# Kernel tuning notes

Hardware: AMD Instinct MI355X
Metric: run time of the kernel (lower is better)

Reference implementation:

```python
import jax, jax.numpy as jnp
import numpy as np

NUM_BINS = 10
BIN_DISP = 0.5
MIN_REG = 1e-5
H = 22
W = 22
S = 16
C = 256
F_ = H * W


def _distance_map(center, sz):
    # DiMP DistanceMap: soft-binned radial distance from center. [bins, sz0, sz1]
    bins = jnp.arange(NUM_BINS, dtype=jnp.float32)[:, None, None]
    k0 = jnp.arange(sz[0], dtype=jnp.float32)[:, None]
    k1 = jnp.arange(sz[1], dtype=jnp.float32)[None, :]
    dist = jnp.sqrt((k0 - center[0]) ** 2 + (k1 - center[1]) ** 2)
    bd = dist[None] / BIN_DISP - bins
    lower = jax.nn.relu(1.0 - jnp.abs(bd[:-1]))
    last = jnp.clip(1.0 + bd[-1:], 0.0, 1.0)
    return jnp.concatenate([lower, last], axis=0)


def _unfold_map(fm, h, w):
    # Equivalent of F.unfold(full_map,(h,w)).view(h,w,h,w).flip((2,3)).permute(2,3,0,1):
    # out[f=(li,lj), ki, kj] = fm[h-1-li+ki, w-1-lj+kj]
    r = (h - 1 - jnp.arange(h))[:, None] + jnp.arange(h)[None, :]  # [li, ki]
    c = (w - 1 - jnp.arange(w))[:, None] + jnp.arange(w)[None, :]  # [lj, kj]
    m = fm[r[:, None, :, None], c[None, :, None, :]]  # [li, lj, ki, kj]
    return m.reshape(h * w, h, w)


def setup_inputs() -> dict:
    key = jax.random.key(0)
    k1, k2 = jax.random.split(key)
    filt = jax.random.normal(k1, (S, F_, C, 1, 1), jnp.float32) * 0.1
    feat = jax.random.normal(k2, (1, S, C, H, W), jnp.float32)
    d = jnp.arange(NUM_BINS, dtype=jnp.float32) * BIN_DISP
    init_gauss = jnp.exp(-0.5 * d ** 2)  # init_gauss_sigma = 1.0
    return {
        "filt": filt,
        "feat": feat,
        "log_step_length": jnp.zeros((1,), jnp.float32),          # log(1.0)
        "filter_reg": 0.01 * jnp.ones((1,), jnp.float32),
        "label_w": init_gauss - init_gauss.min(),                  # label_map_predictor weights
        "mask_w": 4.0 * jnp.tanh(2.0 - d),                         # target_mask_predictor weights
        "spatial_w": jnp.ones((NUM_BINS,), jnp.float32),           # spatial_weight_predictor weights
        "num_iter": 3,
    }


def _forward(filt, feat, log_step_length, filter_reg, label_w, mask_w, spatial_w, num_iter):
    f2 = feat[0]            # [S, C, H, W]
    w = filt[..., 0, 0]     # [S, F, C]   (1x1 DiCor filters)
    h, wd = feat.shape[-2], feat.shape[-1]
    s, fnum = w.shape[0], w.shape[1]
    sz = (2 * h - 1, 2 * wd - 1)
    center = jnp.array([sz[0] // 2, sz[1] // 2], dtype=jnp.float32)
    dmap = _distance_map(center, sz)  # [bins, 2H-1, 2W-1]
    # 1x1 convs over the bin dimension, then unfold into per-filter maps [F, H, W]
    label_map = _unfold_map(jnp.einsum('bhw,b->hw', dmap, label_w), h, wd)
    target_mask = _unfold_map(jax.nn.sigmoid(jnp.einsum('bhw,b->hw', dmap, mask_w)), h, wd)
    spatial_weight = _unfold_map(jnp.einsum('bhw,b->hw', dmap, spatial_w), h, wd)
    step_length = jnp.exp(log_step_length[0])
    reg_weight = jnp.maximum(filter_reg[0] * filter_reg[0], MIN_REG ** 2)
    a = target_mask
    sw2 = spatial_weight * spatial_weight
    for _ in range(num_iter):
        # apply_filter with 1x1 filters: scores[s,f,h,w] = sum_c feat[s,c,h,w] * w[s,f,c]
        scores = jnp.einsum('schw,sfc->sfhw', f2, w)
        # LeakyReluPar / LeakyReluParDeriv with per-location slope a
        scores_act = 0.5 * (1.0 - a) * jnp.abs(scores) + 0.5 * (1.0 + a) * scores
        score_mask = 0.5 * (1.0 - a) * jnp.sign(scores) + 0.5 * (1.0 + a)
        residuals = score_mask * (sw2 * (scores_act - label_map))
        # apply_feat_transpose with 1x1 filters
        w_grad = jnp.einsum('sfhw,schw->sfc', residuals, f2) + reg_weight * w
        scores_grad = jnp.einsum('schw,sfc->sfhw', f2, w_grad)
        scores_grad = spatial_weight * (score_mask * scores_grad)
        alpha_num = jnp.sum(w_grad * w_grad, axis=2)  # [S, F]
        alpha_den = jnp.maximum(
            jnp.sum((scores_grad * scores_grad).reshape(s, fnum, -1), axis=2)
            + reg_weight * alpha_num, 1e-8)
        alpha = alpha_num / alpha_den
        w = w - step_length * alpha[..., None] * w_grad
    return w[..., None, None]  # [S, F, C, 1, 1]


def reference(filt, feat, log_step_length, filter_reg, label_w, mask_w, spatial_w, num_iter):
    return _forward(filt, feat, log_step_length, filter_reg, label_w, mask_w, spatial_w, num_iter)
```

## Files before the change

### kernel.cpp

```cpp
#include <hip/hip_runtime.h>
#include <math.h>
#include <stdint.h>

#define Ww 22
#define P_ 484
#define S_ 16
#define C_ 256
#define MP2 234256
#define TSZ 1849

typedef _Float16 f16x8 __attribute__((ext_vector_type(8)));
typedef _Float16 f16x4 __attribute__((ext_vector_type(4)));
typedef float f32x4 __attribute__((ext_vector_type(4)));

__device__ __forceinline__ void gld16(const _Float16* g, _Float16* lds) {
    auto* lp = (__attribute__((address_space(3))) uint32_t*)(uintptr_t)(lds);
    auto* gp = (const __attribute__((address_space(1))) uint32_t*)(uintptr_t)(g);
    __builtin_amdgcn_global_load_lds(gp, lp, 16, 0, 0);
}

__global__ void k_maps(const float* __restrict__ label_w, const float* __restrict__ mask_w,
                       const float* __restrict__ spatial_w, f32x4* __restrict__ map4t) {
    int idx = blockIdx.x * blockDim.x + threadIdx.x;
    if (idx >= TSZ) return;
    int dx = idx / 43 - 21, dy = idx % 43 - 21;
    float d = sqrtf((float)(dx * dx + dy * dy)) * 2.0f;
    float lab = 0.f, msk = 0.f, spw = 0.f;
#pragma unroll
    for (int b = 0; b < 9; ++b) {
        float wb = fmaxf(0.f, 1.f - fabsf(d - (float)b));
        lab += wb * label_w[b];
        msk += wb * mask_w[b];
        spw += wb * spatial_w[b];
    }
    float w9 = fminf(fmaxf(1.f + (d - 9.f), 0.f), 1.f);
    lab += w9 * label_w[9];
    msk += w9 * mask_w[9];
    spw += w9 * spatial_w[9];
    f32x4 o;
    o[0] = lab;
    o[1] = 1.f / (1.f + expf(-msk));
    o[2] = spw * spw;
    o[3] = spw;
    map4t[idx] = o;
}

__global__ __launch_bounds__(256) void k_winit(const float* __restrict__ filt,
                                               float* __restrict__ Wf, _Float16* __restrict__ Wh,
                                               float* __restrict__ num, float* __restrict__ den) {
    int t = threadIdx.x;
    int f = blockIdx.x * 4 + (t >> 6);
    int s = blockIdx.y;
    int c = (t & 63) * 4;
    size_t oh = ((size_t)(s * 512 + f)) * C_ + c;
    if (f < P_) {
        size_t o = ((size_t)(s * P_ + f)) * C_ + c;
        f32x4 v = *(const f32x4*)(filt + o);
        *(f32x4*)(Wf + o) = v;
        f16x4 h;
#pragma unroll
        for (int q = 0; q < 4; ++q) h[q] = (_Float16)v[q];
        *(f16x4*)(Wh + oh) = h;
        if ((t & 63) == 0) { num[s * P_ + f] = 0.f; den[s * P_ + f] = 0.f; }
    } else {
        f16x4 h = {};
        *(f16x4*)(Wh + oh) = h;
    }
}

__global__ __launch_bounds__(256) void k_trans(const float* __restrict__ feat,
                                               _Float16* __restrict__ f2h,
                                               _Float16* __restrict__ f2th) {
    int s = blockIdx.z;
    int p0 = blockIdx.x * 32, c0 = blockIdx.y * 32;
    int cc = threadIdx.x & 31, rr = threadIdx.x >> 5;
    __shared__ float tb[32][33];
#pragma unroll
    for (int q = 0; q < 4; ++q) {
        int c = c0 + rr + q * 8;
        int p = p0 + cc;
        float v = (p < P_) ? feat[((size_t)s * C_ + c) * P_ + p] : 0.f;
        f2h[((size_t)s * C_ + c) * 512 + p] = (_Float16)v;
        tb[rr + q * 8][cc] = v;
    }
    __syncthreads();
#pragma unroll
    for (int q = 0; q < 4; ++q) {
        int p = p0 + rr + q * 8;
        f2th[((size_t)s * 512 + p) * C_ + c0 + cc] = (_Float16)tb[cc][rr + q * 8];
    }
}

template <int EPI, int KK, int LDA, int LDB>
__global__ __launch_bounds__(256, 4) void k_gemm(
    const _Float16* __restrict__ Ah, const _Float16* __restrict__ Bh,
    const f32x4* __restrict__ map4t, const _Float16* __restrict__ maskh_i,
    const _Float16* __restrict__ Wh_i, const float* __restrict__ freg,
    _Float16* __restrict__ out_h, _Float16* __restrict__ out_h2,
    float* __restrict__ red) {
    constexpr int TI = 2, TJ = 2, NT = KK / 128;
    int tid = threadIdx.x;
    int w = tid >> 6, l = tid & 63;
    int s = blockIdx.x;
    int m0 = blockIdx.y * 64, n0 = blockIdx.z * 64;
    int wm = w >> 1, wn = w & 1;
    int r16 = l & 15;

    __shared__ _Float16 As[64 * 128];
    __shared__ _Float16 Bs[64 * 128];

    int lrow = w * 4 + (l >> 4);
    int gsrc = ((l & 15) ^ lrow) << 3;
    const _Float16* gA = Ah + (size_t)s * (512 * LDA) + (size_t)(m0 + lrow) * LDA + gsrc;
    const _Float16* gB = Bh + (size_t)s * 131072 + (size_t)(n0 + lrow) * LDB + gsrc;

    f32x4 acc[TI][TJ] = {};

#pragma unroll
    for (int t = 0; t < NT; ++t) {
#pragma unroll
        for (int i = 0; i < 4; ++i) {
            gld16(gA + (size_t)i * 16 * LDA + t * 128, &As[(i * 16 + w * 4) * 128]);
            gld16(gB + (size_t)i * 16 * LDB + t * 128, &Bs[(i * 16 + w * 4) * 128]);
        }
        __syncthreads();
#pragma unroll
        for (int kk = 0; kk < 4; ++kk) {
            int px = ((kk * 4 + (l >> 4)) ^ r16) << 3;
            f16x8 af[TI], bf[TJ];
#pragma unroll
            for (int ti = 0; ti < TI; ++ti)
                af[ti] = *(const f16x8*)&As[(wm * 32 + ti * 16 + r16) * 128 + px];
#pragma unroll
            for (int tj = 0; tj < TJ; ++tj)
                bf[tj] = *(const f16x8*)&Bs[(wn * 32 + tj * 16 + r16) * 128 + px];
#pragma unroll
            for (int ti = 0; ti < TI; ++ti)
#pragma unroll
                for (int tj = 0; tj < TJ; ++tj)
                    acc[ti][tj] = __builtin_amdgcn_mfma_f32_16x16x32_f16(
                        af[ti], bf[tj], acc[ti][tj], 0, 0, 0);
        }
        if (t + 1 < NT) __syncthreads();
    }

    int q4 = (l >> 4) * 4;

    if constexpr (EPI == 1) {
#pragma unroll
        for (int ti = 0; ti < TI; ++ti)
#pragma unroll
            for (int r = 0; r < 4; ++r) {
                int m = m0 + wm * 32 + ti * 16 + q4 + r;
                int im = m / 22, jm = m - im * 22;
#pragma unroll
                for (int tj = 0; tj < TJ; ++tj) {
                    int n = n0 + wn * 32 + tj * 16 + r16;
                    float res = 0.f;
                    if (m < P_ && n < P_) {
                        int kn = n / 22, ln = n - kn * 22;
                        f32x4 m4 = map4t[(kn - im + 21) * 43 + (ln - jm + 21)];
                        float sc = acc[ti][tj][r];
                        float sgn = (sc > 0.f) ? 1.f : ((sc < 0.f) ? -1.f : 0.f);
                        float msk = 0.5f * (1.f - m4[1]) * sgn + 0.5f * (1.f + m4[1]);
                        res = msk * (m4[2] * (msk * sc - m4[0]));
                        out_h2[(size_t)s * MP2 + (size_t)m * P_ + n] = (_Float16)msk;
                    }
                    out_h[((size_t)(s * 512 + m)) * 512 + n] = (_Float16)res;
                }
            }
    } else if constexpr (EPI == 2) {
        float fr = freg[0];
        float regw = fmaxf(fr * fr, 1e-10f);
#pragma unroll
        for (int ti = 0; ti < TI; ++ti)
#pragma unroll
            for (int r = 0; r < 4; ++r) {
                int m = m0 + wm * 32 + ti * 16 + q4 + r;
                float v = 0.f;
#pragma unroll
                for (int tj = 0; tj < TJ; ++tj) {
                    int n = n0 + wn * 32 + tj * 16 + r16;
                    size_t o = ((size_t)(s * 512 + m)) * C_ + n;
                    float wg = acc[ti][tj][r] + regw * (float)Wh_i[o];
                    out_h[o] = (_Float16)wg;
                    v += wg * wg;
                }
                v += __shfl_xor(v, 1);
                v += __shfl_xor(v, 2);
                v += __shfl_xor(v, 4);
                v += __shfl_xor(v, 8);
                if (r16 == 0 && m < P_) atomicAdd(&red[s * P_ + m], v);
            }
    } else {
#pragma unroll
        for (int ti = 0; ti < TI; ++ti)
#pragma unroll
            for (int r = 0; r < 4; ++r) {
                int m = m0 + wm * 32 + ti * 16 + q4 + r;
                int im = m / 22, jm = m - im * 22;
                float v = 0.f;
#pragma unroll
                for (int tj = 0; tj < TJ; ++tj) {
                    int n = n0 + wn * 32 + tj * 16 + r16;
                    if (m < P_ && n < P_) {
                        int kn = n / 22, ln = n - kn * 22;
                        float spw = map4t[(kn - im + 21) * 43 + (ln - jm + 21)][3];
                        float msk = (float)maskh_i[(size_t)s * MP2 + (size_t)m * P_ + n];
                        float sg = spw * msk * acc[ti][tj][r];
                        v += sg * sg;
                    }
                }
                v += __shfl_xor(v, 1);
                v += __shfl_xor(v, 2);
                v += __shfl_xor(v, 4);
                v += __shfl_xor(v, 8);
                if (r16 == 0 && m < P_) atomicAdd(&red[s * P_ + m], v);
            }
    }
}

__global__ __launch_bounds__(256) void k_update(float* __restrict__ Wf,
                                                const _Float16* __restrict__ wgradh,
                                                float* __restrict__ num, float* __restrict__ den,
                                                const float* __restrict__ freg,
                                                const float* __restrict__ lsl,
                                                _Float16* __restrict__ Wh) {
    int t = threadIdx.x;
    int f = blockIdx.x * 4 + (t >> 6);
    int s = blockIdx.y;
    int row = s * P_ + f;
    float nu = num[row], de = den[row];
    float fr = freg[0];
    float regw = fmaxf(fr * fr, 1e-10f);
    float alpha = nu / fmaxf(de + regw * nu, 1e-8f);
    float sa = expf(lsl[0]) * alpha;
    int c = (t & 63) * 4;
    size_t o = (size_t)row * C_ + c;
    size_t oh = ((size_t)(s * 512 + f)) * C_ + c;
    f32x4 wv = *(const f32x4*)(Wf + o);
    f16x4 g = *(const f16x4*)(wgradh + oh);
    f16x4 h;
#pragma unroll
    for (int q = 0; q < 4; ++q) {
        wv[q] -= sa * (float)g[q];
        h[q] = (_Float16)wv[q];
    }
    *(f32x4*)(Wf + o) = wv;
    *(f16x4*)(Wh + oh) = h;
    if ((t & 63) == 0) { num[row] = 0.f; den[row] = 0.f; }
}

extern "C" void kernel_launch(void* const* d_in, const int* in_sizes, int n_in,
                              void* d_out, int out_size, void* d_ws, size_t ws_size,
                              hipStream_t stream) {
    const float* filt = (const float*)d_in[0];
    const float* feat = (const float*)d_in[1];
    const float* lsl  = (const float*)d_in[2];
    const float* freg = (const float*)d_in[3];
    const float* lw   = (const float*)d_in[4];
    const float* mw   = (const float*)d_in[5];
    const float* sw   = (const float*)d_in[6];
    float* Wf = (float*)d_out;

    char* ws = (char*)d_ws;
    f32x4* map4t     = (f32x4*)ws;      ws += (size_t)TSZ * 16;
    _Float16* residh = (_Float16*)ws;   ws += (size_t)S_ * 512 * 512 * 2;
    _Float16* wgradh = (_Float16*)ws;   ws += (size_t)S_ * 512 * C_ * 2;
    _Float16* Wh     = (_Float16*)ws;   ws += (size_t)S_ * 512 * C_ * 2;
    _Float16* f2h    = (_Float16*)ws;   ws += (size_t)S_ * C_ * 512 * 2;
    _Float16* f2th   = (_Float16*)ws;   ws += (size_t)S_ * 512 * C_ * 2;
    _Float16* maskh  = (_Float16*)ws;   ws += (size_t)S_ * MP2 * 2;
    float* num       = (float*)ws;      ws += (size_t)S_ * P_ * 4;
    float* den       = (float*)ws;      ws += (size_t)S_ * P_ * 4;

    k_maps<<<8, 256, 0, stream>>>(lw, mw, sw, map4t);
    k_winit<<<dim3(128, S_), 256, 0, stream>>>(filt, Wf, Wh, num, den);
    k_trans<<<dim3(16, 8, S_), 256, 0, stream>>>(feat, f2h, f2th);

    for (int it = 0; it < 3; ++it) {
        k_gemm<1, 256, 256, 256><<<dim3(16, 8, 8), 256, 0, stream>>>(
            Wh, f2th, map4t, nullptr, nullptr, nullptr, residh, maskh, nullptr);
        k_gemm<2, 512, 512, 512><<<dim3(16, 8, 4), 256, 0, stream>>>(
            residh, f2h, map4t, nullptr, Wh, freg, wgradh, nullptr, num);
        k_gemm<3, 256, 256, 256><<<dim3(16, 8, 8), 256, 0, stream>>>(
            wgradh, f2th, map4t, maskh, nullptr, nullptr, nullptr, nullptr, den);
        k_update<<<dim3(121, S_), 256, 0, stream>>>(Wf, wgradh, num, den, freg, lsl, Wh);
    }
}
```

Measured before the change: 146.5 us.

## Update scores by linearity and fuse per-iteration GEMMs into one kernel

```diff
diff --git a/kernel.cpp b/kernel.cpp
--- a/kernel.cpp
+++ b/kernel.cpp
@@ -6,12 +6,15 @@
 #define P_ 484
 #define S_ 16
 #define C_ 256
-#define MP2 234256
 #define TSZ 1849
 
 typedef _Float16 f16x8 __attribute__((ext_vector_type(8)));
 typedef _Float16 f16x4 __attribute__((ext_vector_type(4)));
 typedef float f32x4 __attribute__((ext_vector_type(4)));
+
+__device__ __forceinline__ int xcd_chunk(int bid, int chunk) {
+    return (bid & 7) * chunk + (bid >> 3);
+}
 
 __device__ __forceinline__ void gld16(const _Float16* g, _Float16* lds) {
     auto* lp = (__attribute__((address_space(3))) uint32_t*)(uintptr_t)(lds);
@@ -19,12 +22,8 @@
     __builtin_amdgcn_global_load_lds(gp, lp, 16, 0, 0);
 }
 
-__global__ void k_maps(const float* __restrict__ label_w, const float* __restrict__ mask_w,
-                       const float* __restrict__ spatial_w, f32x4* __restrict__ map4t) {
-    int idx = blockIdx.x * blockDim.x + threadIdx.x;
-    if (idx >= TSZ) return;
-    int dx = idx / 43 - 21, dy = idx % 43 - 21;
-    float d = sqrtf((float)(dx * dx + dy * dy)) * 2.0f;
+__device__ __forceinline__ f32x4 map_entry(const float* label_w, const float* mask_w,
+                                           const float* spatial_w, float d) {
     float lab = 0.f, msk = 0.f, spw = 0.f;
 #pragma unroll
     for (int b = 0; b < 9; ++b) {
@@ -42,67 +41,79 @@
     o[1] = 1.f / (1.f + expf(-msk));
     o[2] = spw * spw;
     o[3] = spw;
-    map4t[idx] = o;
-}
-
-__global__ __launch_bounds__(256) void k_winit(const float* __restrict__ filt,
-                                               float* __restrict__ Wf, _Float16* __restrict__ Wh,
-                                               float* __restrict__ num, float* __restrict__ den) {
+    return o;
+}
+
+__global__ __launch_bounds__(256) void k_pro(
+    const float* __restrict__ filt, const float* __restrict__ feat,
+    const float* __restrict__ lw, const float* __restrict__ mw,
+    const float* __restrict__ sw,
+    float* __restrict__ Wf, _Float16* __restrict__ Wh,
+    _Float16* __restrict__ f2h, _Float16* __restrict__ f2th,
+    f32x4* __restrict__ map4t) {
+    int wgid = xcd_chunk(blockIdx.x, 514);
+    int x = wgid / 514;
+    int local = wgid % 514;
     int t = threadIdx.x;
-    int f = blockIdx.x * 4 + (t >> 6);
-    int s = blockIdx.y;
-    int c = (t & 63) * 4;
-    size_t oh = ((size_t)(s * 512 + f)) * C_ + c;
-    if (f < P_) {
-        size_t o = ((size_t)(s * P_ + f)) * C_ + c;
-        f32x4 v = *(const f32x4*)(filt + o);
-        *(f32x4*)(Wf + o) = v;
-        f16x4 h;
-#pragma unroll
-        for (int q = 0; q < 4; ++q) h[q] = (_Float16)v[q];
-        *(f16x4*)(Wh + oh) = h;
-        if ((t & 63) == 0) { num[s * P_ + f] = 0.f; den[s * P_ + f] = 0.f; }
-    } else {
-        f16x4 h = {};
-        *(f16x4*)(Wh + oh) = h;
-    }
-}
-
-__global__ __launch_bounds__(256) void k_trans(const float* __restrict__ feat,
-                                               _Float16* __restrict__ f2h,
-                                               _Float16* __restrict__ f2th) {
-    int s = blockIdx.z;
-    int p0 = blockIdx.x * 32, c0 = blockIdx.y * 32;
-    int cc = threadIdx.x & 31, rr = threadIdx.x >> 5;
-    __shared__ float tb[32][33];
-#pragma unroll
-    for (int q = 0; q < 4; ++q) {
-        int c = c0 + rr + q * 8;
-        int p = p0 + cc;
-        float v = (p < P_) ? feat[((size_t)s * C_ + c) * P_ + p] : 0.f;
-        f2h[((size_t)s * C_ + c) * 512 + p] = (_Float16)v;
-        tb[rr + q * 8][cc] = v;
-    }
-    __syncthreads();
-#pragma unroll
-    for (int q = 0; q < 4; ++q) {
-        int p = p0 + rr + q * 8;
-        f2th[((size_t)s * 512 + p) * C_ + c0 + cc] = (_Float16)tb[cc][rr + q * 8];
-    }
-}
-
-template <int EPI, int KK, int LDA, int LDB>
-__global__ __launch_bounds__(256, 4) void k_gemm(
+    if (local == 0) {
+        int idx = x + 8 * t;
+        if (idx < TSZ) {
+            int dx = idx / 43 - 21, dy = idx % 43 - 21;
+            float d = sqrtf((float)(dx * dx + dy * dy)) * 2.0f;
+            map4t[idx] = map_entry(lw, mw, sw, d);
+        }
+    } else if (local < 257) {
+        int u = local - 1;
+        int s = x * 2 + (u >> 7);
+        int f = (u & 127) * 4 + (t >> 6);
+        int c = (t & 63) * 4;
+        size_t oh = ((size_t)(s * 512 + f)) * C_ + c;
+        if (f < P_) {
+            size_t o = ((size_t)(s * P_ + f)) * C_ + c;
+            f32x4 v = *(const f32x4*)(filt + o);
+            *(f32x4*)(Wf + o) = v;
+            f16x4 h;
+#pragma unroll
+            for (int q = 0; q < 4; ++q) h[q] = (_Float16)v[q];
+            *(f16x4*)(Wh + oh) = h;
+        } else {
+            f16x4 h = {};
+            *(f16x4*)(Wh + oh) = h;
+        }
+    } else if (local < 513) {
+        int u = local - 257;
+        int s = x * 2 + (u >> 7);
+        int rem = u & 127;
+        int p0 = (rem & 15) * 32, c0 = (rem >> 4) * 32;
+        int cc = t & 31, rr = t >> 5;
+        __shared__ float tb[32][33];
+#pragma unroll
+        for (int q = 0; q < 4; ++q) {
+            int c = c0 + rr + q * 8;
+            int p = p0 + cc;
+            float v = (p < P_) ? feat[((size_t)s * C_ + c) * P_ + p] : 0.f;
+            f2h[((size_t)s * C_ + c) * 512 + p] = (_Float16)v;
+            tb[rr + q * 8][cc] = v;
+        }
+        __syncthreads();
+#pragma unroll
+        for (int q = 0; q < 4; ++q) {
+            int p = p0 + rr + q * 8;
+            f2th[((size_t)s * 512 + p) * C_ + c0 + cc] = (_Float16)tb[cc][rr + q * 8];
+        }
+    }
+}
+
+__global__ __launch_bounds__(256, 4) void k_g1(
     const _Float16* __restrict__ Ah, const _Float16* __restrict__ Bh,
-    const f32x4* __restrict__ map4t, const _Float16* __restrict__ maskh_i,
-    const _Float16* __restrict__ Wh_i, const float* __restrict__ freg,
-    _Float16* __restrict__ out_h, _Float16* __restrict__ out_h2,
-    float* __restrict__ red) {
-    constexpr int TI = 2, TJ = 2, NT = KK / 128;
+    const f32x4* __restrict__ map4t,
+    _Float16* __restrict__ residh, _Float16* __restrict__ scoresh) {
     int tid = threadIdx.x;
     int w = tid >> 6, l = tid & 63;
-    int s = blockIdx.x;
-    int m0 = blockIdx.y * 64, n0 = blockIdx.z * 64;
+    int wgid = xcd_chunk(blockIdx.x, 128);
+    int s = wgid / 64;
+    int rem = wgid % 64;
+    int m0 = (rem / 8) * 64, n0 = (rem % 8) * 64;
     int wm = w >> 1, wn = w & 1;
     int r16 = l & 15;
 
@@ -111,144 +122,268 @@
 
     int lrow = w * 4 + (l >> 4);
     int gsrc = ((l & 15) ^ lrow) << 3;
-    const _Float16* gA = Ah + (size_t)s * (512 * LDA) + (size_t)(m0 + lrow) * LDA + gsrc;
-    const _Float16* gB = Bh + (size_t)s * 131072 + (size_t)(n0 + lrow) * LDB + gsrc;
-
-    f32x4 acc[TI][TJ] = {};
-
-#pragma unroll
-    for (int t = 0; t < NT; ++t) {
+    const _Float16* gA = Ah + (size_t)s * 131072 + (size_t)(m0 + lrow) * 256 + gsrc;
+    const _Float16* gB = Bh + (size_t)s * 131072 + (size_t)(n0 + lrow) * 256 + gsrc;
+
+    f32x4 acc[2][2] = {};
+
+#pragma unroll
+    for (int t = 0; t < 2; ++t) {
 #pragma unroll
         for (int i = 0; i < 4; ++i) {
-            gld16(gA + (size_t)i * 16 * LDA + t * 128, &As[(i * 16 + w * 4) * 128]);
-            gld16(gB + (size_t)i * 16 * LDB + t * 128, &Bs[(i * 16 + w * 4) * 128]);
+            gld16(gA + (size_t)i * 16 * 256 + t * 128, &As[(i * 16 + w * 4) * 128]);
+            gld16(gB + (size_t)i * 16 * 256 + t * 128, &Bs[(i * 16 + w * 4) * 128]);
         }
         __syncthreads();
 #pragma unroll
         for (int kk = 0; kk < 4; ++kk) {
             int px = ((kk * 4 + (l >> 4)) ^ r16) << 3;
-            f16x8 af[TI], bf[TJ];
-#pragma unroll
-            for (int ti = 0; ti < TI; ++ti)
+            f16x8 af[2], bf[2];
+#pragma unroll
+            for (int ti = 0; ti < 2; ++ti)
                 af[ti] = *(const f16x8*)&As[(wm * 32 + ti * 16 + r16) * 128 + px];
 #pragma unroll
-            for (int tj = 0; tj < TJ; ++tj)
+            for (int tj = 0; tj < 2; ++tj)
                 bf[tj] = *(const f16x8*)&Bs[(wn * 32 + tj * 16 + r16) * 128 + px];
 #pragma unroll
-            for (int ti = 0; ti < TI; ++ti)
-#pragma unroll
-                for (int tj = 0; tj < TJ; ++tj)
+            for (int ti = 0; ti < 2; ++ti)
+#pragma unroll
+                for (int tj = 0; tj < 2; ++tj)
                     acc[ti][tj] = __builtin_amdgcn_mfma_f32_16x16x32_f16(
                         af[ti], bf[tj], acc[ti][tj], 0, 0, 0);
         }
-        if (t + 1 < NT) __syncthreads();
+        if (t == 0) __syncthreads();
     }
 
     int q4 = (l >> 4) * 4;
-
-    if constexpr (EPI == 1) {
-#pragma unroll
-        for (int ti = 0; ti < TI; ++ti)
-#pragma unroll
-            for (int r = 0; r < 4; ++r) {
-                int m = m0 + wm * 32 + ti * 16 + q4 + r;
-                int im = m / 22, jm = m - im * 22;
-#pragma unroll
-                for (int tj = 0; tj < TJ; ++tj) {
-                    int n = n0 + wn * 32 + tj * 16 + r16;
-                    float res = 0.f;
-                    if (m < P_ && n < P_) {
-                        int kn = n / 22, ln = n - kn * 22;
-                        f32x4 m4 = map4t[(kn - im + 21) * 43 + (ln - jm + 21)];
-                        float sc = acc[ti][tj][r];
-                        float sgn = (sc > 0.f) ? 1.f : ((sc < 0.f) ? -1.f : 0.f);
-                        float msk = 0.5f * (1.f - m4[1]) * sgn + 0.5f * (1.f + m4[1]);
-                        res = msk * (m4[2] * (msk * sc - m4[0]));
-                        out_h2[(size_t)s * MP2 + (size_t)m * P_ + n] = (_Float16)msk;
-                    }
-                    out_h[((size_t)(s * 512 + m)) * 512 + n] = (_Float16)res;
+#pragma unroll
+    for (int ti = 0; ti < 2; ++ti)
+#pragma unroll
+        for (int r = 0; r < 4; ++r) {
+            int m = m0 + wm * 32 + ti * 16 + q4 + r;
+            int im = m / 22, jm = m - im * 22;
+#pragma unroll
+            for (int tj = 0; tj < 2; ++tj) {
+                int n = n0 + wn * 32 + tj * 16 + r16;
+                float sc = acc[ti][tj][r];
+                float res = 0.f;
+                size_t po = ((size_t)(s * 512 + m)) * 512 + n;
+                if (m < P_ && n < P_) {
+                    int kn = n / 22, ln = n - kn * 22;
+                    f32x4 m4 = map4t[(kn - im + 21) * 43 + (ln - jm + 21)];
+                    float sgn = (sc > 0.f) ? 1.f : ((sc < 0.f) ? -1.f : 0.f);
+                    float msk = 0.5f * (1.f - m4[1]) * sgn + 0.5f * (1.f + m4[1]);
+                    res = msk * (m4[2] * (msk * sc - m4[0]));
                 }
-            }
-    } else if constexpr (EPI == 2) {
-        float fr = freg[0];
-        float regw = fmaxf(fr * fr, 1e-10f);
-#pragma unroll
-        for (int ti = 0; ti < TI; ++ti)
-#pragma unroll
-            for (int r = 0; r < 4; ++r) {
-                int m = m0 + wm * 32 + ti * 16 + q4 + r;
-                float v = 0.f;
-#pragma unroll
-                for (int tj = 0; tj < TJ; ++tj) {
-                    int n = n0 + wn * 32 + tj * 16 + r16;
-                    size_t o = ((size_t)(s * 512 + m)) * C_ + n;
-                    float wg = acc[ti][tj][r] + regw * (float)Wh_i[o];
-                    out_h[o] = (_Float16)wg;
-                    v += wg * wg;
-                }
-                v += __shfl_xor(v, 1);
-                v += __shfl_xor(v, 2);
-                v += __shfl_xor(v, 4);
-                v += __shfl_xor(v, 8);
-                if (r16 == 0 && m < P_) atomicAdd(&red[s * P_ + m], v);
-            }
-    } else {
-#pragma unroll
-        for (int ti = 0; ti < TI; ++ti)
-#pragma unroll
-            for (int r = 0; r < 4; ++r) {
-                int m = m0 + wm * 32 + ti * 16 + q4 + r;
-                int im = m / 22, jm = m - im * 22;
-                float v = 0.f;
-#pragma unroll
-                for (int tj = 0; tj < TJ; ++tj) {
-                    int n = n0 + wn * 32 + tj * 16 + r16;
-                    if (m < P_ && n < P_) {
-                        int kn = n / 22, ln = n - kn * 22;
-                        float spw = map4t[(kn - im + 21) * 43 + (ln - jm + 21)][3];
-                        float msk = (float)maskh_i[(size_t)s * MP2 + (size_t)m * P_ + n];
-                        float sg = spw * msk * acc[ti][tj][r];
-                        v += sg * sg;
-                    }
-                }
-                v += __shfl_xor(v, 1);
-                v += __shfl_xor(v, 2);
-                v += __shfl_xor(v, 4);
-                v += __shfl_xor(v, 8);
-                if (r16 == 0 && m < P_) atomicAdd(&red[s * P_ + m], v);
-            }
-    }
-}
-
-__global__ __launch_bounds__(256) void k_update(float* __restrict__ Wf,
-                                                const _Float16* __restrict__ wgradh,
-                                                float* __restrict__ num, float* __restrict__ den,
-                                                const float* __restrict__ freg,
-                                                const float* __restrict__ lsl,
-                                                _Float16* __restrict__ Wh) {
-    int t = threadIdx.x;
-    int f = blockIdx.x * 4 + (t >> 6);
-    int s = blockIdx.y;
-    int row = s * P_ + f;
-    float nu = num[row], de = den[row];
+                residh[po] = (_Float16)res;
+                scoresh[po] = (_Float16)sc;
+            }
+        }
+}
+
+template <bool LAST>
+__global__ __launch_bounds__(256, 1) void k_iter(
+    _Float16* __restrict__ residh, _Float16* __restrict__ scoresh,
+    const _Float16* __restrict__ f2h, const _Float16* __restrict__ f2th,
+    _Float16* __restrict__ Wh, float* __restrict__ Wf,
+    const f32x4* __restrict__ map4t,
+    const float* __restrict__ freg, const float* __restrict__ lsl) {
+
+    __shared__ _Float16 Bs[128 * 128];
+    __shared__ _Float16 Afull[32 * 512];
+    __shared__ _Float16 Wg[32 * 256];
+    __shared__ _Float16 Sg[32 * 512];
+    __shared__ float num_p[2][32], den_p[2][32], alpha_l[32];
+
+    int tid = threadIdx.x;
+    int w = tid >> 6, l = tid & 63;
+    int wgid = xcd_chunk(blockIdx.x, 32);
+    int s = wgid >> 4;
+    int m0 = (wgid & 15) * 32;
+    int wm = w >> 1, wn = w & 1;
+    int r16 = l & 15;
+    int g4 = l >> 4;
+    int q4 = g4 * 4;
+
     float fr = freg[0];
     float regw = fmaxf(fr * fr, 1e-10f);
-    float alpha = nu / fmaxf(de + regw * nu, 1e-8f);
-    float sa = expf(lsl[0]) * alpha;
-    int c = (t & 63) * 4;
-    size_t o = (size_t)row * C_ + c;
-    size_t oh = ((size_t)(s * 512 + f)) * C_ + c;
-    f32x4 wv = *(const f32x4*)(Wf + o);
-    f16x4 g = *(const f16x4*)(wgradh + oh);
-    f16x4 h;
-#pragma unroll
-    for (int q = 0; q < 4; ++q) {
-        wv[q] -= sa * (float)g[q];
-        h[q] = (_Float16)wv[q];
-    }
-    *(f32x4*)(Wf + o) = wv;
-    *(f16x4*)(Wh + oh) = h;
-    if ((t & 63) == 0) { num[row] = 0.f; den[row] = 0.f; }
+    float step = expf(lsl[0]);
+
+    if (tid < 64) { ((float*)num_p)[tid] = 0.f; ((float*)den_p)[tid] = 0.f; }
+    {
+        const _Float16* src = residh + ((size_t)(s * 512 + m0)) * 512;
+#pragma unroll
+        for (int i = 0; i < 8; ++i) {
+            int row = w * 8 + i;
+            gld16(src + (size_t)row * 512 + ((l ^ (row & 15)) << 3), Afull + row * 512);
+        }
+    }
+    __syncthreads();
+
+#pragma unroll
+    for (int nn = 0; nn < 2; ++nn) {
+        f32x4 acc[4];
+#pragma unroll
+        for (int tj = 0; tj < 4; ++tj) acc[tj] = (f32x4){0.f, 0.f, 0.f, 0.f};
+#pragma unroll
+        for (int t = 0; t < 4; ++t) {
+            const _Float16* src = f2h + (size_t)s * 131072 + (size_t)(nn * 128) * 512 + t * 128;
+#pragma unroll
+            for (int i = 0; i < 8; ++i) {
+                int lr = w * 32 + i * 4 + g4;
+                gld16(src + (size_t)lr * 512 + (((l & 15) ^ (lr & 15)) << 3),
+                      Bs + (w * 32 + i * 4) * 128);
+            }
+            __syncthreads();
+#pragma unroll
+            for (int kk = 0; kk < 4; ++kk) {
+                int pg = ((kk * 4 + g4) ^ r16) << 3;
+                f16x8 af = *(const f16x8*)&Afull[(wm * 16 + r16) * 512 + t * 128 + pg];
+                f16x8 bf[4];
+#pragma unroll
+                for (int tj = 0; tj < 4; ++tj)
+                    bf[tj] = *(const f16x8*)&Bs[(wn * 64 + tj * 16 + r16) * 128 + pg];
+#pragma unroll
+                for (int tj = 0; tj < 4; ++tj)
+                    acc[tj] = __builtin_amdgcn_mfma_f32_16x16x32_f16(af, bf[tj], acc[tj], 0, 0, 0);
+            }
+            __syncthreads();
+        }
+#pragma unroll
+        for (int r = 0; r < 4; ++r) {
+            int m_l = wm * 16 + q4 + r;
+            float v = 0.f;
+#pragma unroll
+            for (int tj = 0; tj < 4; ++tj) {
+                int c = nn * 128 + wn * 64 + tj * 16 + r16;
+                float wg = acc[tj][r] + regw * (float)Wh[((size_t)(s * 512 + m0 + m_l)) * 256 + c];
+                Wg[m_l * 256 + (((c >> 3) ^ (m_l & 15)) << 3) + (c & 7)] = (_Float16)wg;
+                v += wg * wg;
+            }
+            v += __shfl_xor(v, 1); v += __shfl_xor(v, 2);
+            v += __shfl_xor(v, 4); v += __shfl_xor(v, 8);
+            if (r16 == 0) num_p[wn][m_l] += v;
+        }
+    }
+
+#pragma unroll
+    for (int nn2 = 0; nn2 < 4; ++nn2) {
+        f32x4 acc[4];
+#pragma unroll
+        for (int tj = 0; tj < 4; ++tj) acc[tj] = (f32x4){0.f, 0.f, 0.f, 0.f};
+#pragma unroll
+        for (int t2 = 0; t2 < 2; ++t2) {
+            const _Float16* src = f2th + (size_t)s * 131072 + (size_t)(nn2 * 128) * 256 + t2 * 128;
+#pragma unroll
+            for (int i = 0; i < 8; ++i) {
+                int lr = w * 32 + i * 4 + g4;
+                gld16(src + (size_t)lr * 256 + (((l & 15) ^ (lr & 15)) << 3),
+                      Bs + (w * 32 + i * 4) * 128);
+            }
+            __syncthreads();
+#pragma unroll
+            for (int kk = 0; kk < 4; ++kk) {
+                int pg = ((kk * 4 + g4) ^ r16) << 3;
+                f16x8 af = *(const f16x8*)&Wg[(wm * 16 + r16) * 256 + t2 * 128 + pg];
+                f16x8 bf[4];
+#pragma unroll
+                for (int tj = 0; tj < 4; ++tj)
+                    bf[tj] = *(const f16x8*)&Bs[(wn * 64 + tj * 16 + r16) * 128 + pg];
+#pragma unroll
+                for (int tj = 0; tj < 4; ++tj)
+                    acc[tj] = __builtin_amdgcn_mfma_f32_16x16x32_f16(af, bf[tj], acc[tj], 0, 0, 0);
+            }
+            __syncthreads();
+        }
+#pragma unroll
+        for (int r = 0; r < 4; ++r) {
+            int m_l = wm * 16 + q4 + r;
+            int mg = m0 + m_l;
+            int im = mg / 22, jm = mg - im * 22;
+            float v = 0.f;
+#pragma unroll
+            for (int tj = 0; tj < 4; ++tj) {
+                int n = nn2 * 128 + wn * 64 + tj * 16 + r16;
+                float a = acc[tj][r];
+                if (!LAST) Sg[m_l * 512 + n] = (_Float16)a;
+                if (mg < P_ && n < P_) {
+                    float sc = (float)scoresh[((size_t)(s * 512 + mg)) * 512 + n];
+                    int kn = n / 22, ln = n - kn * 22;
+                    f32x4 m4 = map4t[(kn - im + 21) * 43 + (ln - jm + 21)];
+                    float sgn = (sc > 0.f) ? 1.f : ((sc < 0.f) ? -1.f : 0.f);
+                    float msk = 0.5f * (1.f - m4[1]) * sgn + 0.5f * (1.f + m4[1]);
+                    float sg = m4[3] * msk * a;
+                    v += sg * sg;
+                }
+            }
+            v += __shfl_xor(v, 1); v += __shfl_xor(v, 2);
+            v += __shfl_xor(v, 4); v += __shfl_xor(v, 8);
+            if (r16 == 0) den_p[wn][m_l] += v;
+        }
+    }
+    __syncthreads();
+
+    if (tid < 32) {
+        float nu = num_p[0][tid] + num_p[1][tid];
+        float de = den_p[0][tid] + den_p[1][tid];
+        alpha_l[tid] = step * (nu / fmaxf(de + regw * nu, 1e-8f));
+    }
+    __syncthreads();
+
+    int m_l = tid >> 3;
+    int mg = m0 + m_l;
+    float sa = alpha_l[m_l];
+
+    if (!LAST) {
+        int im = mg / 22, jm = mg - im * 22;
+#pragma unroll
+        for (int ch = 0; ch < 8; ++ch) {
+            int col = (tid & 7) * 64 + ch * 8;
+            size_t go = ((size_t)(s * 512 + mg)) * 512 + col;
+            f16x8 so = *(const f16x8*)(scoresh + go);
+            f16x8 sg8 = *(const f16x8*)&Sg[m_l * 512 + col];
+            f16x8 sn, rs;
+#pragma unroll
+            for (int j = 0; j < 8; ++j) {
+                float sc = (float)so[j] - sa * (float)sg8[j];
+                sn[j] = (_Float16)sc;
+                int n = col + j;
+                float res = 0.f;
+                if (mg < P_ && n < P_) {
+                    int kn = n / 22, ln = n - kn * 22;
+                    f32x4 m4 = map4t[(kn - im + 21) * 43 + (ln - jm + 21)];
+                    float sgn = (sc > 0.f) ? 1.f : ((sc < 0.f) ? -1.f : 0.f);
+                    float msk = 0.5f * (1.f - m4[1]) * sgn + 0.5f * (1.f + m4[1]);
+                    res = msk * (m4[2] * (msk * sc - m4[0]));
+                }
+                rs[j] = (_Float16)res;
+            }
+            *(f16x8*)(scoresh + go) = sn;
+            *(f16x8*)(residh + go) = rs;
+        }
+    }
+    if (mg < P_) {
+        int cb = (tid & 7) * 32;
+        int key = m_l & 15;
+        f16x8 wg8[4];
+#pragma unroll
+        for (int jj = 0; jj < 4; ++jj)
+            wg8[jj] = *(const f16x8*)&Wg[m_l * 256 + ((((cb >> 3) + jj) ^ key) << 3)];
+#pragma unroll
+        for (int q = 0; q < 8; ++q) {
+            int c = cb + q * 4;
+            size_t o = ((size_t)(s * P_ + mg)) * 256 + c;
+            f32x4 wv = *(const f32x4*)(Wf + o);
+            f16x4 h;
+#pragma unroll
+            for (int e = 0; e < 4; ++e) {
+                wv[e] -= sa * (float)wg8[q >> 1][(q & 1) * 4 + e];
+                h[e] = (_Float16)wv[e];
+            }
+            *(f32x4*)(Wf + o) = wv;
+            if (!LAST) *(f16x4*)(Wh + ((size_t)(s * 512 + mg)) * 256 + c) = h;
+        }
+    }
 }
 
 extern "C" void kernel_launch(void* const* d_in, const int* in_sizes, int n_in,
@@ -266,25 +401,14 @@
     char* ws = (char*)d_ws;
     f32x4* map4t     = (f32x4*)ws;      ws += (size_t)TSZ * 16;
     _Float16* residh = (_Float16*)ws;   ws += (size_t)S_ * 512 * 512 * 2;
-    _Float16* wgradh = (_Float16*)ws;   ws += (size_t)S_ * 512 * C_ * 2;
+    _Float16* scoresh= (_Float16*)ws;   ws += (size_t)S_ * 512 * 512 * 2;
     _Float16* Wh     = (_Float16*)ws;   ws += (size_t)S_ * 512 * C_ * 2;
     _Float16* f2h    = (_Float16*)ws;   ws += (size_t)S_ * C_ * 512 * 2;
     _Float16* f2th   = (_Float16*)ws;   ws += (size_t)S_ * 512 * C_ * 2;
-    _Float16* maskh  = (_Float16*)ws;   ws += (size_t)S_ * MP2 * 2;
-    float* num       = (float*)ws;      ws += (size_t)S_ * P_ * 4;
-    float* den       = (float*)ws;      ws += (size_t)S_ * P_ * 4;
-
-    k_maps<<<8, 256, 0, stream>>>(lw, mw, sw, map4t);
-    k_winit<<<dim3(128, S_), 256, 0, stream>>>(filt, Wf, Wh, num, den);
-    k_trans<<<dim3(16, 8, S_), 256, 0, stream>>>(feat, f2h, f2th);
-
-    for (int it = 0; it < 3; ++it) {
-        k_gemm<1, 256, 256, 256><<<dim3(16, 8, 8), 256, 0, stream>>>(
-            Wh, f2th, map4t, nullptr, nullptr, nullptr, residh, maskh, nullptr);
-        k_gemm<2, 512, 512, 512><<<dim3(16, 8, 4), 256, 0, stream>>>(
-            residh, f2h, map4t, nullptr, Wh, freg, wgradh, nullptr, num);
-        k_gemm<3, 256, 256, 256><<<dim3(16, 8, 8), 256, 0, stream>>>(
-            wgradh, f2th, map4t, maskh, nullptr, nullptr, nullptr, nullptr, den);
-        k_update<<<dim3(121, S_), 256, 0, stream>>>(Wf, wgradh, num, den, freg, lsl, Wh);
-    }
-}
+
+    k_pro<<<4112, 256, 0, stream>>>(filt, feat, lw, mw, sw, Wf, Wh, f2h, f2th, map4t);
+    k_g1<<<1024, 256, 0, stream>>>(Wh, f2th, map4t, residh, scoresh);
+    k_iter<false><<<256, 256, 0, stream>>>(residh, scoresh, f2h, f2th, Wh, Wf, map4t, freg, lsl);
+    k_iter<false><<<256, 256, 0, stream>>>(residh, scoresh, f2h, f2th, Wh, Wf, map4t, freg, lsl);
+    k_iter<true><<<256, 256, 0, stream>>>(residh, scoresh, f2h, f2th, Wh, Wf, map4t, freg, lsl);
+}
```

Result: slower. 218.4 us (+49.1%).
